# Kernel optimization log

Hardware: AMD Instinct MI355X
Metric: run time of the kernel (lower is better)

## Reference

```python
import jax, jax.numpy as jnp
import numpy as np
from jax import lax


def setup_inputs() -> dict:
    key = jax.random.key(0)
    k1, k2, k3, k4 = jax.random.split(key, 4)
    N, D, B, R, EF = 100000, 256, 64, 32, 32
    storage = jax.random.normal(k1, (N, D), dtype=jnp.float32)
    query = jax.random.normal(k2, (B, D), dtype=jnp.float32)
    graph = jax.random.randint(k3, (N, R), 0, N, dtype=jnp.int32)      # fixed-degree NSW adjacency
    initial = jax.random.randint(k4, (B, EF), 0, N, dtype=jnp.int32)   # random entry points (entry())
    return {"query": query, "storage": storage, "graph": graph,
            "initial": initial, "k": 10, "ef_search": EF}


def reference(query, storage, graph, initial, k, ef_search):
    """Batched greedy best-first NSW search (ef_search fixed expansion steps)."""
    N = storage.shape[0]
    INF = jnp.float32(1e30)

    def sqdist(q, ids):
        diff = storage[ids] - q            # [R, D] gather
        return jnp.sum(diff * diff, axis=-1)

    def search_one(q, init):
        cd = sqdist(q, init)                               # candidate distances [EF]
        visited = jnp.zeros((N,), jnp.bool_).at[init].set(True)
        expanded = jnp.zeros((N,), jnp.bool_)

        def step(state, _):
            cid, cd, visited, expanded = state
            # pick closest unexpanded candidate
            pickd = jnp.where(expanded[cid], INF, cd)
            j = jnp.argmin(pickd)
            u = cid[j]
            expanded = expanded.at[u].set(True)
            # expand neighbors of u
            nbrs = graph[u]                                # [R]
            fresh = ~visited[nbrs]
            nd = jnp.where(fresh, sqdist(q, nbrs), INF)    # skip already-visited
            visited = visited.at[nbrs].set(True)
            # merge candidate pool, keep ef_search best
            all_ids = jnp.concatenate([cid, nbrs])
            all_d = jnp.concatenate([cd, nd])
            negd, idx = lax.top_k(-all_d, ef_search)
            return (all_ids[idx], -negd, visited, expanded), None

        (cid, cd, _, _), _ = lax.scan(step, (init, cd, visited, expanded),
                                      None, length=ef_search)
        negk, idx = lax.top_k(-cd, k)
        return cid[idx], -negk

    topk_ids, topk_dists = jax.vmap(search_one)(query, initial)
    return topk_ids, topk_dists
```

## Files before the change

kernel.cpp:

```cpp
#include <hip/hip_runtime.h>


#define DIMS   256
#define RDEG   32
#define EFPOOL 32
#define KOUT   10
#define NWORDS 3125
#define INF_D  1e30f

typedef unsigned long long u64;

__global__ __launch_bounds__(64, 1) void nsw_wave_kernel(
    const float* __restrict__ query,
    const float* __restrict__ storage,
    const int*   __restrict__ graph,
    const int*   __restrict__ initial,
    float*       __restrict__ out,
    int B)
{
    __shared__ unsigned int visited[NWORDS];
    __shared__ unsigned int expanded[NWORDS];
    __shared__ float4 qsh[DIMS / 4];
    __shared__ float  rows[RDEG * DIMS];
    __shared__ u64    keys[64];
    __shared__ float  sc_d[EFPOOL];
    __shared__ int    sc_id[EFPOOL];

    const int l    = threadIdx.x;
    const int b    = blockIdx.x;
    const int nb   = l & 31;
    const int half = l >> 5;
    const int sw   = nb & 7;

    for (int i = l; i < NWORDS; i += 64) { visited[i] = 0u; expanded[i] = 0u; }

    qsh[l] = reinterpret_cast<const float4*>(query + (size_t)b * DIMS)[l];

    float pool_d  = INF_D;
    int   pool_id = 0;
    int   u       = 0;
    int   nbid    = initial[b * EFPOOL + nb];

    for (int s = 0; s <= EFPOOL; ++s) {
        const bool is_init = (s == 0);

        if (!is_init && l == 0) expanded[u >> 5] |= 1u << (u & 31);

        #pragma unroll
        for (int j = 0; j < RDEG; ++j) {
            int gidj = __shfl(nbid, j, 64);
            const float* src = storage + (size_t)gidj * DIMS + ((l ^ (j & 7)) << 2);
            __builtin_amdgcn_global_load_lds(
                (const __attribute__((address_space(1))) void*)src,
                (__attribute__((address_space(3))) void*)&rows[j * DIMS], 16, 0, 0);
        }

        unsigned vw = visited[nbid >> 5];
        bool fresh = is_init ? true : !((vw >> (nbid & 31)) & 1u);
        if ((l < 32) && fresh) atomicOr(&visited[nbid >> 5], 1u << (nbid & 31));

        asm volatile("s_waitcnt vmcnt(0)" ::: "memory");
        float a0 = 0.f, a1 = 0.f, a2 = 0.f, a3 = 0.f;
        {
            const float4* rp = reinterpret_cast<const float4*>(rows) + nb * 64 + half * 32;
            const float4* qp = qsh + half * 32;
            #pragma unroll
            for (int j = 0; j < 32; ++j) {
                float4 r = rp[j ^ sw];
                float4 q = qp[j];
                float d0 = r.x - q.x; a0 = fmaf(d0, d0, a0);
                float d1 = r.y - q.y; a1 = fmaf(d1, d1, a1);
                float d2 = r.z - q.z; a2 = fmaf(d2, d2, a2);
                float d3 = r.w - q.w; a3 = fmaf(d3, d3, a3);
            }
        }
        float part = (a0 + a1) + (a2 + a3);
        float d  = part + __shfl_xor(part, 32, 64);
        float nd = fresh ? d : INF_D;

        bool eflag = half ? (!fresh)
                          : (((expanded[pool_id >> 5] >> (pool_id & 31)) & 1u) != 0u);
        float ed_e = half ? nd : pool_d;
        u64 ek = ((u64)(eflag ? 1u : 0u) << 62)
               | ((u64)__float_as_uint(ed_e) << 6) | (unsigned)l;
        #pragma unroll
        for (int m = 1; m < 64; m <<= 1) {
            u64 o = __shfl_xor(ek, m, 64);
            ek = (o < ek) ? o : ek;
        }
        int cidx  = (int)(ek & 63);
        int myid  = half ? nbid : pool_id;
        int uspec = __shfl(myid, cidx, 64);

        int nnbid = graph[(size_t)uspec * RDEG + nb];

        {
            float ed  = half ? nd   : pool_d;
            int   eid = half ? nbid : pool_id;
            u64 key = ((u64)__float_as_uint(ed) << 6) | (unsigned)l;
            keys[l] = key;
            int rank = 0;
            #pragma unroll
            for (int j = 0; j < 64; ++j)
                rank += (keys[j] < key) ? 1 : 0;
            if (rank < EFPOOL) { sc_d[rank] = ed; sc_id[rank] = eid; }
            pool_d  = sc_d[nb];
            pool_id = sc_id[nb];
        }

        {
            bool unexp = !((expanded[pool_id >> 5] >> (pool_id & 31)) & 1u);
            u64 bm = __ballot(unexp && (l < 32));
            int slot = (bm == 0ull) ? 0 : (__ffsll(bm) - 1);
            int utrue = sc_id[slot];
            int ut = __builtin_amdgcn_readfirstlane(utrue);
            int us = __builtin_amdgcn_readfirstlane(uspec);
            if (ut != us) {
                nnbid = graph[(size_t)ut * RDEG + nb];
            }
            u = utrue;
        }
        nbid = nnbid;
    }

    if (l < KOUT) {
        out[b * KOUT + l]            = (float)pool_id;
        out[B * KOUT + b * KOUT + l] = pool_d;
    }
}

extern "C" void kernel_launch(void* const* d_in, const int* in_sizes, int n_in,
                              void* d_out, int out_size, void* d_ws, size_t ws_size,
                              hipStream_t stream) {
    const float* query   = (const float*)d_in[0];
    const float* storage = (const float*)d_in[1];
    const int*   graph   = (const int*)d_in[2];
    const int*   initial = (const int*)d_in[3];
    float* out = (float*)d_out;

    const int B = in_sizes[0] / DIMS;

    nsw_wave_kernel<<<B, 64, 0, stream>>>(query, storage, graph, initial, out, B);
}
```

Baseline: 260.0 us.

## Load neighbor rows directly into registers and skip loads for visited neighbors

Drops the async global-to-LDS staging of all 32 neighbor rows. Each lane now loads half of its own neighbor's row straight into registers, and only when that neighbor is fresh, so rows already visited are never fetched. The speculative next-node selection is narrowed to a 32-bit key with truncated distance bits, and it is skipped on the final iteration. This saves memory traffic and LDS space, but each lane now holds a large per-lane register array, the loads are strided per lane instead of coalesced, and the truncated key can misorder close distances in the speculation (the fallback check corrects this).

```diff
diff --git a/kernel.cpp b/kernel.cpp
--- a/kernel.cpp
+++ b/kernel.cpp
@@ -21,7 +21,6 @@
     __shared__ unsigned int visited[NWORDS];
     __shared__ unsigned int expanded[NWORDS];
     __shared__ float4 qsh[DIMS / 4];
-    __shared__ float  rows[RDEG * DIMS];
     __shared__ u64    keys[64];
     __shared__ float  sc_d[EFPOOL];
     __shared__ int    sc_id[EFPOOL];
@@ -30,7 +29,6 @@
     const int b    = blockIdx.x;
     const int nb   = l & 31;
     const int half = l >> 5;
-    const int sw   = nb & 7;
 
     for (int i = l; i < NWORDS; i += 64) { visited[i] = 0u; expanded[i] = 0u; }
 
@@ -46,53 +44,49 @@
 
         if (!is_init && l == 0) expanded[u >> 5] |= 1u << (u & 31);
 
-        #pragma unroll
-        for (int j = 0; j < RDEG; ++j) {
-            int gidj = __shfl(nbid, j, 64);
-            const float* src = storage + (size_t)gidj * DIMS + ((l ^ (j & 7)) << 2);
-            __builtin_amdgcn_global_load_lds(
-                (const __attribute__((address_space(1))) void*)src,
-                (__attribute__((address_space(3))) void*)&rows[j * DIMS], 16, 0, 0);
-        }
-
         unsigned vw = visited[nbid >> 5];
         bool fresh = is_init ? true : !((vw >> (nbid & 31)) & 1u);
         if ((l < 32) && fresh) atomicOr(&visited[nbid >> 5], 1u << (nbid & 31));
 
-        asm volatile("s_waitcnt vmcnt(0)" ::: "memory");
-        float a0 = 0.f, a1 = 0.f, a2 = 0.f, a3 = 0.f;
-        {
-            const float4* rp = reinterpret_cast<const float4*>(rows) + nb * 64 + half * 32;
-            const float4* qp = qsh + half * 32;
+        float part = 0.f;
+        if (fresh) {
+            const float4* sp = reinterpret_cast<const float4*>(
+                storage + (size_t)nbid * DIMS) + half * 32;
+            float4 r[32];
+            #pragma unroll
+            for (int j = 0; j < 32; ++j) r[j] = sp[j];
+            float a0 = 0.f, a1 = 0.f, a2 = 0.f, a3 = 0.f;
             #pragma unroll
             for (int j = 0; j < 32; ++j) {
-                float4 r = rp[j ^ sw];
-                float4 q = qp[j];
-                float d0 = r.x - q.x; a0 = fmaf(d0, d0, a0);
-                float d1 = r.y - q.y; a1 = fmaf(d1, d1, a1);
-                float d2 = r.z - q.z; a2 = fmaf(d2, d2, a2);
-                float d3 = r.w - q.w; a3 = fmaf(d3, d3, a3);
+                float4 q = qsh[half * 32 + j];
+                float d0 = r[j].x - q.x; a0 = fmaf(d0, d0, a0);
+                float d1 = r[j].y - q.y; a1 = fmaf(d1, d1, a1);
+                float d2 = r[j].z - q.z; a2 = fmaf(d2, d2, a2);
+                float d3 = r[j].w - q.w; a3 = fmaf(d3, d3, a3);
             }
+            part = (a0 + a1) + (a2 + a3);
         }
-        float part = (a0 + a1) + (a2 + a3);
         float d  = part + __shfl_xor(part, 32, 64);
         float nd = fresh ? d : INF_D;
 
-        bool eflag = half ? (!fresh)
-                          : (((expanded[pool_id >> 5] >> (pool_id & 31)) & 1u) != 0u);
-        float ed_e = half ? nd : pool_d;
-        u64 ek = ((u64)(eflag ? 1u : 0u) << 62)
-               | ((u64)__float_as_uint(ed_e) << 6) | (unsigned)l;
-        #pragma unroll
-        for (int m = 1; m < 64; m <<= 1) {
-            u64 o = __shfl_xor(ek, m, 64);
-            ek = (o < ek) ? o : ek;
+        int nnbid = nbid;
+        int uspec = -1;
+        if (s < EFPOOL) {
+            bool eflag = half ? (!fresh)
+                              : (((expanded[pool_id >> 5] >> (pool_id & 31)) & 1u) != 0u);
+            float ed_e = half ? nd : pool_d;
+            unsigned ek = ((eflag ? 1u : 0u) << 31)
+                        | ((__float_as_uint(ed_e) >> 13) << 6) | (unsigned)l;
+            #pragma unroll
+            for (int m = 1; m < 64; m <<= 1) {
+                unsigned o = __shfl_xor((int)ek, m, 64);
+                ek = (o < ek) ? o : ek;
+            }
+            int cidx  = (int)(ek & 63);
+            int myid  = half ? nbid : pool_id;
+            uspec = __shfl(myid, cidx, 64);
+            nnbid = graph[(size_t)uspec * RDEG + nb];
         }
-        int cidx  = (int)(ek & 63);
-        int myid  = half ? nbid : pool_id;
-        int uspec = __shfl(myid, cidx, 64);
-
-        int nnbid = graph[(size_t)uspec * RDEG + nb];
 
         {
             float ed  = half ? nd   : pool_d;
@@ -108,7 +102,7 @@
             pool_id = sc_id[nb];
         }
 
-        {
+        if (s < EFPOOL) {
             bool unexp = !((expanded[pool_id >> 5] >> (pool_id & 31)) & 1u);
             u64 bm = __ballot(unexp && (l < 32));
             int slot = (bm == 0ull) ? 0 : (__ffsll(bm) - 1);
```

After: 243.1 us. 6.5% less time.

## Drop speculative next-node prefetch and use full XOR LDS swizzle with readlane

Applied to the files above, without the earlier changes.

Removes the speculative argmin reduction that predicted the next expanded node and prefetched its graph row before the pool merge. The graph row is now fetched only after the true next node is known, and that fetch is skipped on the final step. The row layout changes to a float4 array with a full XOR-by-neighbour swizzle, and readlane replaces the shuffle when broadcasting neighbour ids. This removes a 64-lane u64 butterfly reduction per step, but the graph load latency now sits on the critical path.

```diff
diff --git a/kernel.cpp b/kernel.cpp
--- a/kernel.cpp
+++ b/kernel.cpp
@@ -21,7 +21,7 @@
     __shared__ unsigned int visited[NWORDS];
     __shared__ unsigned int expanded[NWORDS];
     __shared__ float4 qsh[DIMS / 4];
-    __shared__ float  rows[RDEG * DIMS];
+    __shared__ float4 rows[RDEG * (DIMS / 4)];
     __shared__ u64    keys[64];
     __shared__ float  sc_d[EFPOOL];
     __shared__ int    sc_id[EFPOOL];
@@ -30,7 +30,6 @@
     const int b    = blockIdx.x;
     const int nb   = l & 31;
     const int half = l >> 5;
-    const int sw   = nb & 7;
 
     for (int i = l; i < NWORDS; i += 64) { visited[i] = 0u; expanded[i] = 0u; }
 
@@ -41,6 +40,8 @@
     int   u       = 0;
     int   nbid    = initial[b * EFPOOL + nb];
 
+    const int vboff = l << 4;
+
     for (int s = 0; s <= EFPOOL; ++s) {
         const bool is_init = (s == 0);
 
@@ -48,11 +49,13 @@
 
         #pragma unroll
         for (int j = 0; j < RDEG; ++j) {
-            int gidj = __shfl(nbid, j, 64);
-            const float* src = storage + (size_t)gidj * DIMS + ((l ^ (j & 7)) << 2);
+            int gid = __builtin_amdgcn_readlane(nbid, j);
+            const char* src = (const char*)(storage + (size_t)gid * DIMS)
+                            + (vboff ^ (j << 4));
             __builtin_amdgcn_global_load_lds(
                 (const __attribute__((address_space(1))) void*)src,
-                (__attribute__((address_space(3))) void*)&rows[j * DIMS], 16, 0, 0);
+                (__attribute__((address_space(3))) void*)&rows[j * (DIMS / 4)],
+                16, 0, 0);
         }
 
         unsigned vw = visited[nbid >> 5];
@@ -62,11 +65,11 @@
         asm volatile("s_waitcnt vmcnt(0)" ::: "memory");
         float a0 = 0.f, a1 = 0.f, a2 = 0.f, a3 = 0.f;
         {
-            const float4* rp = reinterpret_cast<const float4*>(rows) + nb * 64 + half * 32;
+            const float4* rp = rows + nb * (DIMS / 4);
             const float4* qp = qsh + half * 32;
             #pragma unroll
             for (int j = 0; j < 32; ++j) {
-                float4 r = rp[j ^ sw];
+                float4 r = rp[(half * 32 + j) ^ nb];
                 float4 q = qp[j];
                 float d0 = r.x - q.x; a0 = fmaf(d0, d0, a0);
                 float d1 = r.y - q.y; a1 = fmaf(d1, d1, a1);
@@ -77,22 +80,6 @@
         float part = (a0 + a1) + (a2 + a3);
         float d  = part + __shfl_xor(part, 32, 64);
         float nd = fresh ? d : INF_D;
-
-        bool eflag = half ? (!fresh)
-                          : (((expanded[pool_id >> 5] >> (pool_id & 31)) & 1u) != 0u);
-        float ed_e = half ? nd : pool_d;
-        u64 ek = ((u64)(eflag ? 1u : 0u) << 62)
-               | ((u64)__float_as_uint(ed_e) << 6) | (unsigned)l;
-        #pragma unroll
-        for (int m = 1; m < 64; m <<= 1) {
-            u64 o = __shfl_xor(ek, m, 64);
-            ek = (o < ek) ? o : ek;
-        }
-        int cidx  = (int)(ek & 63);
-        int myid  = half ? nbid : pool_id;
-        int uspec = __shfl(myid, cidx, 64);
-
-        int nnbid = graph[(size_t)uspec * RDEG + nb];
 
         {
             float ed  = half ? nd   : pool_d;
@@ -108,19 +95,13 @@
             pool_id = sc_id[nb];
         }
 
-        {
+        if (s < EFPOOL) {
             bool unexp = !((expanded[pool_id >> 5] >> (pool_id & 31)) & 1u);
             u64 bm = __ballot(unexp && (l < 32));
             int slot = (bm == 0ull) ? 0 : (__ffsll(bm) - 1);
-            int utrue = sc_id[slot];
-            int ut = __builtin_amdgcn_readfirstlane(utrue);
-            int us = __builtin_amdgcn_readfirstlane(uspec);
-            if (ut != us) {
-                nnbid = graph[(size_t)ut * RDEG + nb];
-            }
-            u = utrue;
+            u = sc_id[slot];
+            nbid = graph[(size_t)u * RDEG + nb];
         }
-        nbid = nnbid;
     }
 
     if (l < KOUT) {
```

Result: faster. 242.0 us (-6.9%).
